# Kernel optimization log

Measured on AMD Instinct MI355X. Metric: run time of the kernel, lower is better.

Reference implementation:

```python
import jax, jax.numpy as jnp
import numpy as np

NUM_REQS = 8192
MAX_NUM_REQS = 16384
NUM_TOKENS = 16_777_216
MAX_CTX = 32768


def setup_inputs() -> dict:
    key = jax.random.key(0)
    k1, k2, k3 = jax.random.split(key, 3)
    # cumulative query start offsets: sorted, qsl[0]=0, qsl[-1]=NUM_TOKENS
    inner = jnp.sort(jax.random.randint(k1, (NUM_REQS - 1,), 0, NUM_TOKENS, dtype=jnp.int32))
    query_start_loc = jnp.concatenate([
        jnp.zeros((1,), jnp.int32), inner, jnp.full((1,), NUM_TOKENS, jnp.int32)
    ])
    idx_mapping = jax.random.randint(k2, (NUM_REQS,), 0, MAX_NUM_REQS, dtype=jnp.int32)
    num_computed_tokens = jax.random.randint(k3, (MAX_NUM_REQS,), 0, MAX_CTX, dtype=jnp.int32)
    pos = jnp.zeros((NUM_TOKENS,), jnp.int32)       # output buffer
    seq_lens = jnp.zeros((MAX_NUM_REQS,), jnp.int32)  # output buffer
    return {
        "idx_mapping": idx_mapping,
        "query_start_loc": query_start_loc,
        "num_computed_tokens": num_computed_tokens,
        "pos": pos,
        "seq_lens": seq_lens,
    }


def reference(idx_mapping, query_start_loc, num_computed_tokens, pos, seq_lens):
    num_reqs = idx_mapping.shape[0]            # static
    max_num_reqs = seq_lens.shape[0]           # static
    num_tokens = pos.shape[0]                  # static; == query_start_loc[-1] by construction

    # per-request query lengths and gathered computed-token counts
    query_lens = query_start_loc[1:] - query_start_loc[:-1]      # [num_reqs]
    nct = num_computed_tokens[idx_mapping]                       # [num_reqs]

    # seq_lens: [0:num_reqs] = nct + query_len, [num_reqs:] = 0
    seq_lens_out = jnp.zeros((max_num_reqs,), seq_lens.dtype).at[:num_reqs].set(
        (nct + query_lens).astype(seq_lens.dtype)
    )

    # pos: for each token t, find its owning request via searchsorted over
    # the ragged offsets, then pos[t] = nct[req] + (t - start[req]).
    t = jnp.arange(num_tokens, dtype=query_start_loc.dtype)      # [num_tokens]
    req = jnp.searchsorted(query_start_loc, t, side="right") - 1 # [num_tokens]
    req = jnp.clip(req, 0, num_reqs - 1)
    pos_out = (nct[req] + (t - query_start_loc[req])).astype(pos.dtype)

    return pos_out, seq_lens_out
```

## Files before the change

kernel.cpp:

```cpp
#include <hip/hip_runtime.h>


#define TPB 256
#define CHUNKS 8
#define TOK_PER_BLOCK (TPB * 4 * CHUNKS)
#define SEQ_PER_BLOCK (TPB * 4)

__global__ __launch_bounds__(TPB) void pos_seq_kernel(
    const int* __restrict__ idx_mapping,
    const int* __restrict__ qsl,
    const int* __restrict__ nct,
    int* __restrict__ pos_out,
    int* __restrict__ seq_out,
    int num_reqs, int max_num_reqs, int num_tokens,
    int pos_blocks)
{
    int b = blockIdx.x;

    if (b >= pos_blocks) {
        int i = (b - pos_blocks) * SEQ_PER_BLOCK + (int)threadIdx.x * 4;
        if (i >= max_num_reqs) return;
        if (i + 4 <= max_num_reqs) {
            int4 v;
            int* vp = (int*)&v;
            #pragma unroll
            for (int k = 0; k < 4; ++k) {
                int idx = i + k;
                int val = 0;
                if (idx < num_reqs)
                    val = nct[idx_mapping[idx]] + (qsl[idx + 1] - qsl[idx]);
                vp[k] = val;
            }
            *(int4*)(seq_out + i) = v;
        } else {
            for (int idx = i; idx < max_num_reqs; ++idx) {
                int val = 0;
                if (idx < num_reqs)
                    val = nct[idx_mapping[idx]] + (qsl[idx + 1] - qsl[idx]);
                seq_out[idx] = val;
            }
        }
        return;
    }

    long long blockStartL = (long long)b * TOK_PER_BLOCK;
    int blockStart = (int)blockStartL;
    int tid = (int)threadIdx.x;
    int tfirst = blockStart + tid * 4;
    if (tfirst >= num_tokens) return;

    int l = 0, h = num_reqs + 1;
    while (h - l > 1) {
        int mid = (l + h) >> 1;
        if (qsl[mid] <= tfirst) l = mid; else h = mid;
    }
    int r = l;
    int next = qsl[r + 1];
    int base = nct[idx_mapping[r]] - qsl[r];

    #pragma unroll
    for (int g = 0; g < CHUNKS; ++g) {
        int tc = blockStart + g * (TPB * 4) + tid * 4;
        if (tc >= num_tokens) break;
        int4 v;
        int* vp = (int*)&v;
        int t = tc;
        #pragma unroll
        for (int k = 0; k < 4; ++k) {
            while (t >= next) {
                ++r;
                next = qsl[r + 1];
                base = nct[idx_mapping[r]] - qsl[r];
            }
            vp[k] = base + t;
            ++t;
        }
        if (tc + 4 <= num_tokens) {
            *(int4*)(pos_out + tc) = v;
        } else {
            for (int k = 0; k < num_tokens - tc; ++k) pos_out[tc + k] = vp[k];
        }
    }
}

extern "C" void kernel_launch(void* const* d_in, const int* in_sizes, int n_in,
                              void* d_out, int out_size, void* d_ws, size_t ws_size,
                              hipStream_t stream) {
    const int* idx_mapping = (const int*)d_in[0];
    const int* qsl         = (const int*)d_in[1];
    const int* nct         = (const int*)d_in[2];

    int num_reqs     = in_sizes[0];
    int max_num_reqs = in_sizes[2];
    int num_tokens   = in_sizes[3];

    int* out = (int*)d_out;
    int* pos_out = out;
    int* seq_out = out + num_tokens;

    int pos_blocks = (num_tokens + TOK_PER_BLOCK - 1) / TOK_PER_BLOCK;
    int seq_blocks = (max_num_reqs + SEQ_PER_BLOCK - 1) / SEQ_PER_BLOCK;

    dim3 grid(pos_blocks + seq_blocks), block(TPB);
    pos_seq_kernel<<<grid, block, 0, stream>>>(
        idx_mapping, qsl, nct, pos_out, seq_out,
        num_reqs, max_num_reqs, num_tokens, pos_blocks);
}
```

Baseline: 142.5 us.

## Precompute per-tile request index in a prep kernel, shrink pos tiles

Splits the work into two kernels. A prep kernel runs one binary search per 2048-token tile, stores the owning request in workspace, and also fills seq_lens. The pos kernel then starts from that stored index and walks forward, instead of every thread binary-searching over qsl. Tiles go from 8 chunks to 2 per block, which makes many more blocks. The cost is a second launch and a dependency between the two kernels.

After: 143.8 us. Within noise of the previous version (+0.9%).

```diff
diff --git a/kernel.cpp b/kernel.cpp
--- a/kernel.cpp
+++ b/kernel.cpp
@@ -2,66 +2,86 @@
 
 
 #define TPB 256
-#define CHUNKS 8
-#define TOK_PER_BLOCK (TPB * 4 * CHUNKS)
+#define TILE_TOK 2048
 #define SEQ_PER_BLOCK (TPB * 4)
 
-__global__ __launch_bounds__(TPB) void pos_seq_kernel(
+__global__ __launch_bounds__(TPB) void prep_kernel(
     const int* __restrict__ idx_mapping,
     const int* __restrict__ qsl,
     const int* __restrict__ nct,
-    int* __restrict__ pos_out,
+    int* __restrict__ tile_req,
     int* __restrict__ seq_out,
     int num_reqs, int max_num_reqs, int num_tokens,
-    int pos_blocks)
+    int num_tiles, int tile_blocks)
 {
     int b = blockIdx.x;
-
-    if (b >= pos_blocks) {
-        int i = (b - pos_blocks) * SEQ_PER_BLOCK + (int)threadIdx.x * 4;
-        if (i >= max_num_reqs) return;
-        if (i + 4 <= max_num_reqs) {
-            int4 v;
-            int* vp = (int*)&v;
-            #pragma unroll
-            for (int k = 0; k < 4; ++k) {
-                int idx = i + k;
-                int val = 0;
-                if (idx < num_reqs)
-                    val = nct[idx_mapping[idx]] + (qsl[idx + 1] - qsl[idx]);
-                vp[k] = val;
-            }
-            *(int4*)(seq_out + i) = v;
-        } else {
-            for (int idx = i; idx < max_num_reqs; ++idx) {
-                int val = 0;
-                if (idx < num_reqs)
-                    val = nct[idx_mapping[idx]] + (qsl[idx + 1] - qsl[idx]);
-                seq_out[idx] = val;
-            }
+    if (b < tile_blocks) {
+        int tile = b * TPB + (int)threadIdx.x;
+        if (tile >= num_tiles) return;
+        long long tl = (long long)tile * TILE_TOK;
+        int t = (tl >= num_tokens) ? (num_tokens - 1) : (int)tl;
+        int l = 0, h = num_reqs + 1;
+        while (h - l > 1) {
+            int mid = (l + h) >> 1;
+            if (qsl[mid] <= t) l = mid; else h = mid;
         }
+        tile_req[tile] = l;
         return;
     }
+    int i = (b - tile_blocks) * SEQ_PER_BLOCK + (int)threadIdx.x * 4;
+    if (i >= max_num_reqs) return;
+    if (i + 4 <= max_num_reqs) {
+        int4 v;
+        int* vp = (int*)&v;
+        #pragma unroll
+        for (int k = 0; k < 4; ++k) {
+            int idx = i + k;
+            int val = 0;
+            if (idx < num_reqs)
+                val = nct[idx_mapping[idx]] + (qsl[idx + 1] - qsl[idx]);
+            vp[k] = val;
+        }
+        *(int4*)(seq_out + i) = v;
+    } else {
+        for (int idx = i; idx < max_num_reqs; ++idx) {
+            int val = 0;
+            if (idx < num_reqs)
+                val = nct[idx_mapping[idx]] + (qsl[idx + 1] - qsl[idx]);
+            seq_out[idx] = val;
+        }
+    }
+}
 
-    long long blockStartL = (long long)b * TOK_PER_BLOCK;
-    int blockStart = (int)blockStartL;
+__global__ __launch_bounds__(TPB) void pos_kernel(
+    const int* __restrict__ idx_mapping,
+    const int* __restrict__ qsl,
+    const int* __restrict__ nct,
+    const int* __restrict__ tile_req,
+    int* __restrict__ pos_out,
+    int num_reqs, int num_tokens)
+{
+    int tile = blockIdx.x;
+    long long bsl = (long long)tile * TILE_TOK;
+    int blockStart = (int)bsl;
     int tid = (int)threadIdx.x;
+
     int tfirst = blockStart + tid * 4;
     if (tfirst >= num_tokens) return;
 
-    int l = 0, h = num_reqs + 1;
-    while (h - l > 1) {
-        int mid = (l + h) >> 1;
-        if (qsl[mid] <= tfirst) l = mid; else h = mid;
-    }
-    int r = l;
+    int r = tile_req[tile];
     int next = qsl[r + 1];
     int base = nct[idx_mapping[r]] - qsl[r];
 
+    while (tfirst >= next) {
+        ++r;
+        next = qsl[r + 1];
+        base = nct[idx_mapping[r]] - qsl[r];
+    }
+
     #pragma unroll
-    for (int g = 0; g < CHUNKS; ++g) {
+    for (int g = 0; g < 2; ++g) {
         int tc = blockStart + g * (TPB * 4) + tid * 4;
-        if (tc >= num_tokens) break;
+        if (tc >= num_tokens) return;
         int4 v;
         int* vp = (int*)&v;
         int t = tc;
@@ -97,12 +117,16 @@
     int* out = (int*)d_out;
     int* pos_out = out;
     int* seq_out = out + num_tokens;
+    int* tile_req = (int*)d_ws;
 
-    int pos_blocks = (num_tokens + TOK_PER_BLOCK - 1) / TOK_PER_BLOCK;
-    int seq_blocks = (max_num_reqs + SEQ_PER_BLOCK - 1) / SEQ_PER_BLOCK;
+    int num_tiles   = (int)(((long long)num_tokens + TILE_TOK - 1) / TILE_TOK);
+    int tile_blocks = (num_tiles + TPB - 1) / TPB;
+    int seq_blocks  = (max_num_reqs + SEQ_PER_BLOCK - 1) / SEQ_PER_BLOCK;
 
-    dim3 grid(pos_blocks + seq_blocks), block(TPB);
-    pos_seq_kernel<<<grid, block, 0, stream>>>(
-        idx_mapping, qsl, nct, pos_out, seq_out,
-        num_reqs, max_num_reqs, num_tokens, pos_blocks);
+    prep_kernel<<<dim3(tile_blocks + seq_blocks), dim3(TPB), 0, stream>>>(
+        idx_mapping, qsl, nct, tile_req, seq_out,
+        num_reqs, max_num_reqs, num_tokens, num_tiles, tile_blocks);
+
+    pos_kernel<<<dim3(num_tiles), dim3(TPB), 0, stream>>>(
+        idx_mapping, qsl, nct, tile_req, pos_out, num_reqs, num_tokens);
 }
```
